# Performance work log

Measured on AMD Instinct MI355X. Metric: run time of the kernel, lower is better.

## Reference

```python
import jax, jax.numpy as jnp
import numpy as np

B, S, DIM, HEADS, DH = 1, 192, 512, 8, 64
LN_EPS = 1e-5


def setup_inputs() -> dict:
    key = jax.random.key(0)
    ks = jax.random.split(key, 5)
    rn = lambda k, shp: jax.random.normal(k, shp, dtype=jnp.float32) * 0.02
    return {
        "x": jax.random.normal(ks[0], (B, S, DIM), dtype=jnp.float32),
        "ln_w": jnp.ones((DIM,), jnp.float32),
        "ln_b": jnp.zeros((DIM,), jnp.float32),
        "W_abcde": rn(ks[1], (5 * HEADS * DH, DIM)),
        "b_abcde": jnp.zeros((5 * HEADS * DH,), jnp.float32),
        "W_K": rn(ks[2], (HEADS, DH, DH, DH)),
        "W_V": rn(ks[3], (HEADS, DH, DH, DH)),
        "W_out": rn(ks[4], (DIM, HEADS * DH)),
        "b_out": jnp.zeros((DIM,), jnp.float32),
    }


def reference(x, ln_w, ln_b, W_abcde, b_abcde, W_K, W_V, W_out, b_out):
    b, n, _ = x.shape
    # LayerNorm (biased variance, eps=1e-5, affine)
    mu = jnp.mean(x, axis=-1, keepdims=True)
    var = jnp.var(x, axis=-1, keepdims=True)
    xn = (x - mu) / jnp.sqrt(var + LN_EPS) * ln_w + ln_b
    # abcde projection, chunk into 5, split heads -> [b, n, h, d]
    proj = xn @ W_abcde.T + b_abcde
    a_, b_, c_, d_, e_ = [t.reshape(b, n, HEADS, DH) for t in jnp.split(proj, 5, axis=-1)]
    # cubic attention score chain (note: heads summed out in step2, reintroduced by a_)
    step1 = jnp.einsum('brnk,nijk->brij', c_, W_K)          # [b, r, d, d]
    step2 = jnp.einsum('brij,bqnj->briq', step1, b_)        # [b, r, d, q] (sum over heads of b_)
    attn = jnp.einsum('briq,bpni->bnpqr', step2, a_)        # [b, h, p, q, r]
    # "causal" mask: positions where p >= q set to 1e-6 (faithful to masked_fill_)
    t_idx = jnp.arange(n)[:, None, None]
    s_idx = jnp.arange(n)[None, :, None]
    mask = (t_idx >= s_idx)[None, None]                      # [1,1,p,q,1]
    attn = jnp.where(mask, jnp.float32(1e-6), attn)
    # 'b n p1 p2 p3 -> b n p3 (p1 p2)', scale by 1/dim_head, softmax over (p1 p2)
    attn = attn.transpose(0, 1, 4, 2, 3).reshape(b, HEADS, n, n * n) / DH
    attn = jax.nn.softmax(attn, axis=-1)
    # pairwise values: [b, p1, p2, h, d] -> 'b p s n h -> b n h (p s)'
    v = jnp.einsum('bpnh,bqng,nhgf->bpqnf', d_, e_, W_V)
    v = v.transpose(0, 3, 4, 1, 2).reshape(b, HEADS, DH, n * n)
    # weighted sum over pair axis, merge heads
    z = jnp.einsum('bnql,bnhl->bqnh', attn, v).reshape(b, n, HEADS * DH)
    return z @ W_out.T + b_out
```

## Files before the change

kernel.cpp:

```cpp
#include <hip/hip_runtime.h>
#include <hip/hip_bf16.h>
#include <cstdint>

#define SEQ 192

typedef float f32x4 __attribute__((ext_vector_type(4)));
typedef float f32x8 __attribute__((ext_vector_type(8)));
typedef __bf16 bf16;
typedef __bf16 bf16x8 __attribute__((ext_vector_type(8)));
typedef __bf16 bf16x4 __attribute__((ext_vector_type(4)));

#define MFMA_BF16(a, b, c) __builtin_amdgcn_mfma_f32_16x16x32_bf16(a, b, c, 0, 0, 0)

__device__ __forceinline__ bf16x8 cvt8(f32x8 v) {
  bf16x8 o;
#pragma unroll
  for (int i = 0; i < 8; i++) o[i] = (bf16)v[i];
  return o;
}

__global__ __launch_bounds__(256) void k1_prep(
    const float* __restrict__ x, const float* __restrict__ ln_w, const float* __restrict__ ln_b,
    const float* __restrict__ WV, bf16* __restrict__ xn_bf, bf16* __restrict__ WVt2) {
  int bid = blockIdx.x, tid = threadIdx.x;
  if (bid < 512) {
    int g = bid & 63, hh = bid >> 6;
    __shared__ float ld[64 * 65];
    int f = tid & 63, r4 = tid >> 6;
#pragma unroll
    for (int it = 0; it < 16; it++) {
      int hp = it * 4 + r4;
      ld[hp * 65 + f] = WV[(((size_t)(hh * 64 + hp) * 64 + g) * 64) + f];
    }
    __syncthreads();
    int hp2 = tid & 63;
#pragma unroll
    for (int it = 0; it < 16; it++) {
      int ff = it * 4 + r4;
      WVt2[(size_t)hh * 262144 + (size_t)(ff * 64 + g) * 64 + hp2] = (bf16)ld[hp2 * 65 + ff];
    }
    return;
  }
  bid -= 512;
  {
    int r = bid;
    const float* xr = x + (size_t)r * 512;
    float v0 = xr[tid], v1 = xr[tid + 256];
    float s = v0 + v1, s2 = v0 * v0 + v1 * v1;
#pragma unroll
    for (int off = 32; off > 0; off >>= 1) {
      s += __shfl_down(s, off);
      s2 += __shfl_down(s2, off);
    }
    __shared__ float redS[4], redS2[4];
    int wave = tid >> 6, lane = tid & 63;
    if (lane == 0) { redS[wave] = s; redS2[wave] = s2; }
    __syncthreads();
    float S = redS[0] + redS[1] + redS[2] + redS[3];
    float S2 = redS2[0] + redS2[1] + redS2[2] + redS2[3];
    float mean = S * (1.0f / 512.0f);
    float var = S2 * (1.0f / 512.0f) - mean * mean;
    float rstd = rsqrtf(var + 1e-5f);
    bf16* xnr = xn_bf + (size_t)r * 512;
    xnr[tid] = (bf16)((v0 - mean) * rstd * ln_w[tid] + ln_b[tid]);
    xnr[tid + 256] = (bf16)((v1 - mean) * rstd * ln_w[tid + 256] + ln_b[tid + 256]);
  }
}

template <int MODE>
__device__ __forceinline__ void gemm_body(const bf16* __restrict__ A, const bf16* __restrict__ Bt,
                                          bf16* __restrict__ C1, int N, int K,
                                          int nb, int mb, int tid) {
  int n0 = nb * 64, m0 = mb * 64;
  int wave = tid >> 6, lane = tid & 63;
  int lq = lane >> 4, l16 = lane & 15;
  const bf16* Ap = A + (size_t)(m0 + wave * 16 + l16) * K;
  f32x4 acc[4];
#pragma unroll
  for (int nt = 0; nt < 4; nt++) acc[nt] = (f32x4){0.f, 0.f, 0.f, 0.f};
  for (int k0 = 0; k0 < K; k0 += 32) {
    bf16x8 af = *(const bf16x8*)(Ap + k0 + lq * 8);
#pragma unroll
    for (int nt = 0; nt < 4; nt++) {
      bf16x8 bv = *(const bf16x8*)(Bt + (size_t)(n0 + nt * 16 + l16) * K + k0 + lq * 8);
      acc[nt] = MFMA_BF16(af, bv, acc[nt]);
    }
  }
  int cm = m0 + wave * 16 + lq * 4;
#pragma unroll
  for (int nt = 0; nt < 4; nt++) {
    int n = n0 + nt * 16 + l16;
    if constexpr (MODE == 1) {
#pragma unroll
      for (int rg = 0; rg < 4; rg++) C1[(size_t)(cm + rg) * N + n] = (bf16)acc[nt][rg];
    } else {
      int r = cm >> 6, i0 = cm & 63;
      bf16x4 pk = {(bf16)acc[nt][0], (bf16)acc[nt][1], (bf16)acc[nt][2], (bf16)acc[nt][3]};
      *(bf16x4*)(C1 + (size_t)r * 12288 + (size_t)n * 64 + i0) = pk;
    }
  }
}

__global__ __launch_bounds__(256) void k2_proj(
    const bf16* __restrict__ xn_bf, const float* __restrict__ Wab,
    const float* __restrict__ b_abcde, float* __restrict__ proj, bf16* __restrict__ a_bf,
    bf16* __restrict__ c_bf, bf16* __restrict__ d_bf) {
  int bid = blockIdx.x, tid = threadIdx.x;
  int nb = bid % 40, mb = bid / 40;
  int n0 = nb * 64, m0 = mb * 64;
  int wave = tid >> 6, lane = tid & 63;
  int lq = lane >> 4, l16 = lane & 15;
  const bf16* Ap = xn_bf + (size_t)(m0 + wave * 16 + l16) * 512;
  f32x4 acc[4];
#pragma unroll
  for (int nt = 0; nt < 4; nt++) acc[nt] = (f32x4){0.f, 0.f, 0.f, 0.f};
  for (int k0 = 0; k0 < 512; k0 += 32) {
    bf16x8 af = *(const bf16x8*)(Ap + k0 + lq * 8);
#pragma unroll
    for (int nt = 0; nt < 4; nt++) {
      f32x8 wv = *(const f32x8*)(Wab + (size_t)(n0 + nt * 16 + l16) * 512 + k0 + lq * 8);
      acc[nt] = MFMA_BF16(af, cvt8(wv), acc[nt]);
    }
  }
  int cm = m0 + wave * 16 + lq * 4;
#pragma unroll
  for (int nt = 0; nt < 4; nt++) {
    int n = n0 + nt * 16 + l16;
    int chunk = n >> 9, hcol = (n >> 6) & 7, i = n & 63;
#pragma unroll
    for (int rg = 0; rg < 4; rg++) {
      int m = cm + rg;
      float v = acc[nt][rg] + b_abcde[n];
      proj[(size_t)m * 2560 + n] = v;
      bf16 bv = (bf16)v;
      if (chunk == 0) a_bf[((size_t)hcol * SEQ + m) * 64 + i] = bv;
      else if (chunk == 2) c_bf[(size_t)m * 512 + (n - 1024)] = bv;
      else if (chunk == 3) d_bf[((size_t)hcol * SEQ + m) * 64 + i] = bv;
    }
  }
}

__global__ __launch_bounds__(256) void k3_mid(
    const bf16* __restrict__ c_bf, const float* __restrict__ WK, bf16* __restrict__ s1bf,
    const bf16* __restrict__ d_bf, const bf16* __restrict__ WVt2, bf16* __restrict__ tTt,
    const float* __restrict__ proj, bf16* __restrict__ eT_bf, float* __restrict__ ecum,
    bf16* __restrict__ bsum_bf) {
  __shared__ float el[64 * 65];
  int bid = blockIdx.x, tid = threadIdx.x;
  if (bid < 192) {
    int nb = bid % 64, mb = bid / 64;
    int n0 = nb * 64, m0 = mb * 64;
    int wave = tid >> 6, lane = tid & 63;
    int lq = lane >> 4, l16 = lane & 15;
    const bf16* Ap = c_bf + (size_t)(m0 + wave * 16 + l16) * 512;
    f32x4 acc[4];
#pragma unroll
    for (int nt = 0; nt < 4; nt++) acc[nt] = (f32x4){0.f, 0.f, 0.f, 0.f};
    size_t offn[4];
#pragma unroll
    for (int nt = 0; nt < 4; nt++) {
      int n = n0 + nt * 16 + l16;
      offn[nt] = (size_t)(n >> 6) * 4096 + (size_t)(n & 63) * 64;
    }
    for (int k0 = 0; k0 < 512; k0 += 32) {
      bf16x8 af = *(const bf16x8*)(Ap + k0 + lq * 8);
      size_t kb = (size_t)(k0 >> 6) * 262144 + (k0 & 32) + lq * 8;
#pragma unroll
      for (int nt = 0; nt < 4; nt++) {
        f32x8 wv = *(const f32x8*)(WK + kb + offn[nt]);
        acc[nt] = MFMA_BF16(af, cvt8(wv), acc[nt]);
      }
    }
    int cm = m0 + wave * 16 + lq * 4;
#pragma unroll
    for (int nt = 0; nt < 4; nt++) {
      int n = n0 + nt * 16 + l16;
#pragma unroll
      for (int rg = 0; rg < 4; rg++) s1bf[(size_t)(cm + rg) * 4096 + n] = (bf16)acc[nt][rg];
    }
    return;
  }
  bid -= 192;
  if (bid < 1536) {
    int h = bid / 192, rem = bid % 192;
    gemm_body<1>(d_bf + (size_t)h * 12288, WVt2 + (size_t)h * 262144,
                 tTt + (size_t)h * 786432, 4096, 64, rem % 64, rem / 64, tid);
    return;
  }
  bid -= 1536;
  if (bid < 8) {
    int h = bid;
    float carry = 0.f;
    for (int ch = 0; ch < 3; ch++) {
      int pbase = ch * 64;
      for (int idx = tid; idx < 4096; idx += 256) {
        int pl = idx >> 6, g = idx & 63;
        el[pl * 65 + g] = proj[(size_t)(pbase + pl) * 2560 + 2048 + h * 64 + g];
      }
      __syncthreads();
      for (int idx = tid; idx < 4096; idx += 256) {
        int g = idx >> 6, ql = idx & 63;
        eT_bf[((size_t)h * 64 + g) * SEQ + pbase + ql] = (bf16)el[ql * 65 + g];
      }
      if (tid < 64) {
        float run = carry;
        for (int pl = 0; pl < 64; pl++) {
          run += el[pl * 65 + tid];
          ecum[(size_t)h * 12288 + (pbase + pl) * 64 + tid] = run;
        }
        carry = run;
      }
      __syncthreads();
    }
    return;
  }
  bid -= 8;
  {
    int j = tid & 63, qg = tid >> 6;
#pragma unroll
    for (int qi = 0; qi < 16; qi++) {
      int q = bid * 64 + qg * 16 + qi;
      float s = 0.f;
#pragma unroll
      for (int hh = 0; hh < 8; hh++) s += proj[(size_t)q * 2560 + 512 + hh * 64 + j];
      bsum_bf[q * 64 + j] = (bf16)s;
    }
  }
}

__global__ __launch_bounds__(256) void k4_step2(const bf16* __restrict__ s1bf,
                                                const bf16* __restrict__ bsum_bf,
                                                bf16* __restrict__ s2bf) {
  int bid = blockIdx.x;
  gemm_body<2>(s1bf, bsum_bf, s2bf, 192, 64, bid % 3, bid / 3, threadIdx.x);
}

__global__ __launch_bounds__(256, 3) void k5_attn(
    const bf16* __restrict__ a_bf, const bf16* __restrict__ s2bf,
    const bf16* __restrict__ eT_bf, const float* __restrict__ ecum,
    bf16* __restrict__ ew_bf, float* __restrict__ Lsum) {
  int r = blockIdx.x, h = blockIdx.y;
  int tid = threadIdx.x, wave = tid >> 6, lane = tid & 63;
  int lq = lane >> 4, l16 = lane & 15;
  __shared__ __align__(16) bf16 wch[2][4][3][16 * 40];
  __shared__ float redL[4];
  int pt[3] = {wave, wave + 4, 11 - wave};

  const bf16* ah = a_bf + (size_t)h * 12288;
  const bf16* s2r = s2bf + (size_t)r * 12288;
  const bf16* eh = eT_bf + (size_t)h * 12288;
  const float* ech = ecum + (size_t)h * 12288;

  bf16x8 afr[3][2];
#pragma unroll
  for (int mt = 0; mt < 3; mt++)
#pragma unroll
    for (int kc = 0; kc < 2; kc++)
      afr[mt][kc] = *(const bf16x8*)(ah + (pt[mt] * 16 + l16) * 64 + kc * 32 + lq * 8);

  f32x4 ewacc[3][4];
#pragma unroll
  for (int mt = 0; mt < 3; mt++)
#pragma unroll
    for (int nt = 0; nt < 4; nt++) ewacc[mt][nt] = (f32x4){0.f, 0.f, 0.f, 0.f};
  float lpart = 0.f;

  for (int c = 0; c < 6; c++) {
    if (c * 32 + 31 <= wave * 16) continue;
    int par = c & 1;
    bf16x8 efr[4];
#pragma unroll
    for (int nt = 0; nt < 4; nt++)
      efr[nt] = *(const bf16x8*)(eh + (nt * 16 + l16) * SEQ + c * 32 + lq * 8);
    bf16x8 bq[2][2];
#pragma unroll
    for (int sub = 0; sub < 2; sub++) {
      int q = c * 32 + sub * 16 + l16;
      bq[sub][0] = *(const bf16x8*)(s2r + q * 64 + lq * 8);
      bq[sub][1] = *(const bf16x8*)(s2r + q * 64 + 32 + lq * 8);
    }
    f32x4 sacc[3][2];
#pragma unroll
    for (int mt = 0; mt < 3; mt++) {
      if (c * 32 + 31 <= pt[mt] * 16) continue;
#pragma unroll
      for (int sub = 0; sub < 2; sub++) {
        if (c * 32 + sub * 16 + 15 <= pt[mt] * 16) continue;
        f32x4 sv = (f32x4){0.f, 0.f, 0.f, 0.f};
        sv = MFMA_BF16(afr[mt][0], bq[sub][0], sv);
        sacc[mt][sub] = MFMA_BF16(afr[mt][1], bq[sub][1], sv);
      }
    }
#pragma unroll
    for (int mt = 0; mt < 3; mt++) {
      if (c * 32 + 31 <= pt[mt] * 16) continue;
      bf16* mybuf = &wch[par][wave][mt][0];
#pragma unroll
      for (int sub = 0; sub < 2; sub++) {
        if (c * 32 + sub * 16 + 15 <= pt[mt] * 16) {
#pragma unroll
          for (int rg = 0; rg < 4; rg++) mybuf[(lq * 4 + rg) * 40 + sub * 16 + l16] = (bf16)0.f;
          continue;
        }
        int q = c * 32 + sub * 16 + l16;
        int p0 = pt[mt] * 16 + lq * 4;
#pragma unroll
        for (int rg = 0; rg < 4; rg++) {
          float wv = (q > p0 + rg) ? __expf(sacc[mt][sub][rg] * 0.015625f) : 0.f;
          lpart += wv;
          mybuf[(lq * 4 + rg) * 40 + sub * 16 + l16] = (bf16)wv;
        }
      }
    }
#pragma unroll
    for (int mt = 0; mt < 3; mt++) {
      if (c * 32 + 31 <= pt[mt] * 16) continue;
      bf16x8 wf = *(const bf16x8*)(&wch[par][wave][mt][l16 * 40 + lq * 8]);
#pragma unroll
      for (int nt = 0; nt < 4; nt++) ewacc[mt][nt] = MFMA_BF16(wf, efr[nt], ewacc[mt][nt]);
    }
  }

  bf16* ewout = ew_bf + ((size_t)h * SEQ + r) * 12288;
#pragma unroll
  for (int mt = 0; mt < 3; mt++)
#pragma unroll
    for (int nt = 0; nt < 4; nt++)
#pragma unroll
      for (int rg = 0; rg < 4; rg++) {
        int p = pt[mt] * 16 + lq * 4 + rg;
        int g = nt * 16 + l16;
        ewout[p * 64 + g] = (bf16)(ewacc[mt][nt][rg] + ech[p * 64 + g]);
      }

#pragma unroll
  for (int off = 32; off > 0; off >>= 1) lpart += __shfl_down(lpart, off);
  if (lane == 0) redL[wave] = lpart;
  __syncthreads();
  if (tid == 0) Lsum[h * SEQ + r] = redL[0] + redL[1] + redL[2] + redL[3];
}

__global__ __launch_bounds__(512) void k5b_z(
    const bf16* __restrict__ ew_bf, const bf16* __restrict__ tTt, float* __restrict__ Zpart) {
  int h = blockIdx.x, mt = blockIdx.y, ks = blockIdx.z;
  int tid = threadIdx.x, wave = tid >> 6, lane = tid & 63;
  int lq = lane >> 4, l16 = lane & 15;
  __shared__ float zred[8][16][66];
  const bf16* ewh = ew_bf + ((size_t)h * SEQ + mt * 32) * 12288;
  const bf16* th = tTt + (size_t)h * 786432;
  f32x4 acc[2][4];
#pragma unroll
  for (int m2 = 0; m2 < 2; m2++)
#pragma unroll
    for (int nt = 0; nt < 4; nt++) acc[m2][nt] = (f32x4){0.f, 0.f, 0.f, 0.f};
  for (int jj = 0; jj < 6; jj++) {
    int kc = ks * 48 + wave * 6 + jj;
    int p = kc >> 1, g0 = (kc & 1) * 32;
    bf16x8 af0 = *(const bf16x8*)(ewh + (size_t)l16 * 12288 + kc * 32 + lq * 8);
    bf16x8 af1 = *(const bf16x8*)(ewh + (size_t)(16 + l16) * 12288 + kc * 32 + lq * 8);
#pragma unroll
    for (int nt = 0; nt < 4; nt++) {
      bf16x8 tf = *(const bf16x8*)(th + (size_t)p * 4096 + (nt * 16 + l16) * 64 + g0 + lq * 8);
      acc[0][nt] = MFMA_BF16(af0, tf, acc[0][nt]);
      acc[1][nt] = MFMA_BF16(af1, tf, acc[1][nt]);
    }
  }
#pragma unroll
  for (int m2 = 0; m2 < 2; m2++) {
    if (m2) __syncthreads();
#pragma unroll
    for (int nt = 0; nt < 4; nt++)
#pragma unroll
      for (int rg = 0; rg < 4; rg++) zred[wave][lq * 4 + rg][nt * 16 + l16] = acc[m2][nt][rg];
    __syncthreads();
#pragma unroll
    for (int o = 0; o < 2; o++) {
      int idx = o * 512 + tid;
      int rloc = idx >> 6, f = idx & 63;
      float s = 0.f;
#pragma unroll
      for (int wv = 0; wv < 8; wv++) s += zred[wv][rloc][f];
      Zpart[(size_t)ks * 98304 + (size_t)(mt * 32 + m2 * 16 + rloc) * 512 + h * 64 + f] = s;
    }
  }
}

__global__ __launch_bounds__(256) void k5c_zf(const float* __restrict__ Zpart,
                                              const float* __restrict__ Lsum,
                                              bf16* __restrict__ z_bf) {
  int m = blockIdx.x, tid = threadIdx.x;
#pragma unroll
  for (int o = 0; o < 2; o++) {
    int c = o * 256 + tid;
    int h = c >> 6;
    float s = 0.f;
#pragma unroll
    for (int ks = 0; ks < 8; ks++) s += Zpart[(size_t)ks * 98304 + (size_t)m * 512 + c];
    float L = Lsum[h * SEQ + m] + 18528.0f;
    z_bf[(size_t)m * 512 + c] = (bf16)(s / L);
  }
}

__global__ __launch_bounds__(256) void k6_out(
    const bf16* __restrict__ z_bf, const float* __restrict__ Wout,
    const float* __restrict__ b_out, float* __restrict__ out) {
  int bid = blockIdx.x, tid = threadIdx.x;
  int nb = bid & 7, mb = bid >> 3;
  int wave = tid >> 6, lane = tid & 63;
  int lq = lane >> 4, l16 = lane & 15;
  int m = mb * 16 + l16;
  f32x4 acc[4];
#pragma unroll
  for (int nt = 0; nt < 4; nt++) acc[nt] = (f32x4){0.f, 0.f, 0.f, 0.f};
#pragma unroll
  for (int kc = 0; kc < 4; kc++) {
    int k0 = wave * 128 + kc * 32;
    bf16x8 af = *(const bf16x8*)(z_bf + (size_t)m * 512 + k0 + lq * 8);
#pragma unroll
    for (int nt = 0; nt < 4; nt++) {
      f32x8 wv = *(const f32x8*)(Wout + (size_t)(nb * 64 + nt * 16 + l16) * 512 + k0 + lq * 8);
      acc[nt] = MFMA_BF16(af, cvt8(wv), acc[nt]);
    }
  }
  __shared__ float red[4][16][68];
#pragma unroll
  for (int nt = 0; nt < 4; nt++)
#pragma unroll
    for (int rg = 0; rg < 4; rg++) red[wave][lq * 4 + rg][nt * 16 + l16] = acc[nt][rg];
  __syncthreads();
#pragma unroll
  for (int o = 0; o < 4; o++) {
    int idx = o * 256 + tid;
    int rloc = idx >> 6, f = idx & 63;
    float s = red[0][rloc][f] + red[1][rloc][f] + red[2][rloc][f] + red[3][rloc][f];
    out[(size_t)(mb * 16 + rloc) * 512 + nb * 64 + f] = s + b_out[nb * 64 + f];
  }
}

static const size_t OFF_PROJ = 0;
static const size_t OFF_ECUM = 491520;
static const size_t OFF_XN = 589824;
static const size_t OFF_ZPART = 638976;
static const size_t OFF_LSUM = 1425408;
static const size_t OFF_Z = 1427456;
static const size_t OFF_WVT = 2473984;
static const size_t OFF_A = 3522560;
static const size_t OFF_C = 3571712;
static const size_t OFF_D = 3620864;
static const size_t OFF_ET = 3670016;
static const size_t OFF_BSUM = 3719168;
static const size_t OFF_S1 = 3725312;
static const size_t OFF_S2 = 4118528;
static const size_t OFF_TT = 5298176;
static const size_t OFF_EW = 8493056;

extern "C" void kernel_launch(void* const* d_in, const int* in_sizes, int n_in,
                              void* d_out, int out_size, void* d_ws, size_t ws_size,
                              hipStream_t stream) {
  (void)in_sizes; (void)n_in; (void)out_size; (void)ws_size;
  const float* x = (const float*)d_in[0];
  const float* ln_w = (const float*)d_in[1];
  const float* ln_b = (const float*)d_in[2];
  const float* W_abcde = (const float*)d_in[3];
  const float* b_abcde = (const float*)d_in[4];
  const float* W_K = (const float*)d_in[5];
  const float* W_V = (const float*)d_in[6];
  const float* W_out = (const float*)d_in[7];
  const float* b_out = (const float*)d_in[8];
  float* out = (float*)d_out;
  float* ws = (float*)d_ws;

  float* proj = ws + OFF_PROJ;
  float* ecum = ws + OFF_ECUM;
  bf16* xn_bf = (bf16*)(ws + OFF_XN);
  float* Zpart = ws + OFF_ZPART;
  float* Lsum = ws + OFF_LSUM;
  bf16* z_bf = (bf16*)(ws + OFF_Z);
  bf16* WVt2 = (bf16*)(ws + OFF_WVT);
  bf16* a_bf = (bf16*)(ws + OFF_A);
  bf16* c_bf = (bf16*)(ws + OFF_C);
  bf16* d_bf = (bf16*)(ws + OFF_D);
  bf16* eT_bf = (bf16*)(ws + OFF_ET);
  bf16* bsum_bf = (bf16*)(ws + OFF_BSUM);
  bf16* s1bf = (bf16*)(ws + OFF_S1);
  bf16* s2bf = (bf16*)(ws + OFF_S2);
  bf16* tTt = (bf16*)(ws + OFF_TT);
  bf16* ew_bf = (bf16*)(ws + OFF_EW);

  k1_prep<<<704, 256, 0, stream>>>(x, ln_w, ln_b, W_V, xn_bf, WVt2);
  k2_proj<<<120, 256, 0, stream>>>(xn_bf, W_abcde, b_abcde, proj, a_bf, c_bf, d_bf);
  k3_mid<<<1739, 256, 0, stream>>>(c_bf, W_K, s1bf, d_bf, WVt2, tTt, proj, eT_bf, ecum,
                                   bsum_bf);
  k4_step2<<<576, 256, 0, stream>>>(s1bf, bsum_bf, s2bf);
  k5_attn<<<dim3(SEQ, 8), 256, 0, stream>>>(a_bf, s2bf, eT_bf, ecum, ew_bf, Lsum);
  k5b_z<<<dim3(8, 6, 8), 512, 0, stream>>>(ew_bf, tTt, Zpart);
  k5c_zf<<<SEQ, 256, 0, stream>>>(Zpart, Lsum, z_bf);
  k6_out<<<96, 256, 0, stream>>>(z_bf, W_out, b_out, out);
}
```

Before: 214.9 us.

## Fuse step2 GEMM into attention kernel and z-normalize into output projection

Recomputes the s1×bsum step2 product per (r,h) block directly into shared memory inside the attention kernel, removing the separate step2 kernel and its global s2 buffer. Also merges the Zpart reduction/normalization into the output projection kernel, staging z in LDS. This cuts two launches and intermediate global traffic at the cost of redundant step2 work across heads, extra LDS per block, and dropping the double-buffered weight chunk. A missing barrier in the ecum chunk loop is also added.

```diff
diff --git a/kernel.cpp b/kernel.cpp
--- a/kernel.cpp
+++ b/kernel.cpp
@@ -67,10 +67,9 @@
   }
 }
 
-template <int MODE>
-__device__ __forceinline__ void gemm_body(const bf16* __restrict__ A, const bf16* __restrict__ Bt,
-                                          bf16* __restrict__ C1, int N, int K,
-                                          int nb, int mb, int tid) {
+__device__ __forceinline__ void gemm_rm(const bf16* __restrict__ A, const bf16* __restrict__ Bt,
+                                        bf16* __restrict__ C1, int N, int K, int nb, int mb,
+                                        int tid) {
   int n0 = nb * 64, m0 = mb * 64;
   int wave = tid >> 6, lane = tid & 63;
   int lq = lane >> 4, l16 = lane & 15;
@@ -90,14 +89,8 @@
 #pragma unroll
   for (int nt = 0; nt < 4; nt++) {
     int n = n0 + nt * 16 + l16;
-    if constexpr (MODE == 1) {
-#pragma unroll
-      for (int rg = 0; rg < 4; rg++) C1[(size_t)(cm + rg) * N + n] = (bf16)acc[nt][rg];
-    } else {
-      int r = cm >> 6, i0 = cm & 63;
-      bf16x4 pk = {(bf16)acc[nt][0], (bf16)acc[nt][1], (bf16)acc[nt][2], (bf16)acc[nt][3]};
-      *(bf16x4*)(C1 + (size_t)r * 12288 + (size_t)n * 64 + i0) = pk;
-    }
+#pragma unroll
+    for (int rg = 0; rg < 4; rg++) C1[(size_t)(cm + rg) * N + n] = (bf16)acc[nt][rg];
   }
 }
 
@@ -183,8 +176,8 @@
   bid -= 192;
   if (bid < 1536) {
     int h = bid / 192, rem = bid % 192;
-    gemm_body<1>(d_bf + (size_t)h * 12288, WVt2 + (size_t)h * 262144,
-                 tTt + (size_t)h * 786432, 4096, 64, rem % 64, rem / 64, tid);
+    gemm_rm(d_bf + (size_t)h * 12288, WVt2 + (size_t)h * 262144,
+            tTt + (size_t)h * 786432, 4096, 64, rem % 64, rem / 64, tid);
     return;
   }
   bid -= 1536;
@@ -193,6 +186,7 @@
     float carry = 0.f;
     for (int ch = 0; ch < 3; ch++) {
       int pbase = ch * 64;
+      if (ch) __syncthreads();
       for (int idx = tid; idx < 4096; idx += 256) {
         int pl = idx >> 6, g = idx & 63;
         el[pl * 65 + g] = proj[(size_t)(pbase + pl) * 2560 + 2048 + h * 64 + g];
@@ -228,26 +222,39 @@
   }
 }
 
-__global__ __launch_bounds__(256) void k4_step2(const bf16* __restrict__ s1bf,
-                                                const bf16* __restrict__ bsum_bf,
-                                                bf16* __restrict__ s2bf) {
-  int bid = blockIdx.x;
-  gemm_body<2>(s1bf, bsum_bf, s2bf, 192, 64, bid % 3, bid / 3, threadIdx.x);
-}
-
-__global__ __launch_bounds__(256, 3) void k5_attn(
-    const bf16* __restrict__ a_bf, const bf16* __restrict__ s2bf,
-    const bf16* __restrict__ eT_bf, const float* __restrict__ ecum,
-    bf16* __restrict__ ew_bf, float* __restrict__ Lsum) {
+__global__ __launch_bounds__(256, 3) void k45_attn(
+    const bf16* __restrict__ a_bf, const bf16* __restrict__ s1bf,
+    const bf16* __restrict__ bsum_bf, const bf16* __restrict__ eT_bf,
+    const float* __restrict__ ecum, bf16* __restrict__ ew_bf, float* __restrict__ Lsum) {
   int r = blockIdx.x, h = blockIdx.y;
   int tid = threadIdx.x, wave = tid >> 6, lane = tid & 63;
   int lq = lane >> 4, l16 = lane & 15;
-  __shared__ __align__(16) bf16 wch[2][4][3][16 * 40];
+  __shared__ __align__(16) bf16 s2L[SEQ * 72];
+  __shared__ __align__(16) bf16 wch[4][3][16 * 40];
   __shared__ float redL[4];
+
+  {
+    const bf16* s1r = s1bf + (size_t)r * 4096;
+    bf16x8 aS[2];
+#pragma unroll
+    for (int kc = 0; kc < 2; kc++)
+      aS[kc] = *(const bf16x8*)(s1r + (wave * 16 + l16) * 64 + kc * 32 + lq * 8);
+#pragma unroll
+    for (int qt = 0; qt < 12; qt++) {
+      f32x4 acc = (f32x4){0.f, 0.f, 0.f, 0.f};
+#pragma unroll
+      for (int kc = 0; kc < 2; kc++) {
+        bf16x8 bv = *(const bf16x8*)(bsum_bf + (qt * 16 + l16) * 64 + kc * 32 + lq * 8);
+        acc = MFMA_BF16(aS[kc], bv, acc);
+      }
+      bf16x4 pk = {(bf16)acc[0], (bf16)acc[1], (bf16)acc[2], (bf16)acc[3]};
+      *(bf16x4*)(&s2L[(qt * 16 + l16) * 72 + wave * 16 + lq * 4]) = pk;
+    }
+  }
+  __syncthreads();
+
   int pt[3] = {wave, wave + 4, 11 - wave};
-
   const bf16* ah = a_bf + (size_t)h * 12288;
-  const bf16* s2r = s2bf + (size_t)r * 12288;
   const bf16* eh = eT_bf + (size_t)h * 12288;
   const float* ech = ecum + (size_t)h * 12288;
 
@@ -265,27 +272,26 @@
     for (int nt = 0; nt < 4; nt++) ewacc[mt][nt] = (f32x4){0.f, 0.f, 0.f, 0.f};
   float lpart = 0.f;
 
-  for (int c = 0; c < 6; c++) {
-    if (c * 32 + 31 <= wave * 16) continue;
-    int par = c & 1;
+  for (int cc = 0; cc < 6; cc++) {
+    if (cc * 32 + 31 <= wave * 16) continue;
     bf16x8 efr[4];
 #pragma unroll
     for (int nt = 0; nt < 4; nt++)
-      efr[nt] = *(const bf16x8*)(eh + (nt * 16 + l16) * SEQ + c * 32 + lq * 8);
+      efr[nt] = *(const bf16x8*)(eh + (nt * 16 + l16) * SEQ + cc * 32 + lq * 8);
     bf16x8 bq[2][2];
 #pragma unroll
     for (int sub = 0; sub < 2; sub++) {
-      int q = c * 32 + sub * 16 + l16;
-      bq[sub][0] = *(const bf16x8*)(s2r + q * 64 + lq * 8);
-      bq[sub][1] = *(const bf16x8*)(s2r + q * 64 + 32 + lq * 8);
+      int q = cc * 32 + sub * 16 + l16;
+      bq[sub][0] = *(const bf16x8*)(&s2L[q * 72 + lq * 8]);
+      bq[sub][1] = *(const bf16x8*)(&s2L[q * 72 + 32 + lq * 8]);
     }
     f32x4 sacc[3][2];
 #pragma unroll
     for (int mt = 0; mt < 3; mt++) {
-      if (c * 32 + 31 <= pt[mt] * 16) continue;
+      if (cc * 32 + 31 <= pt[mt] * 16) continue;
 #pragma unroll
       for (int sub = 0; sub < 2; sub++) {
-        if (c * 32 + sub * 16 + 15 <= pt[mt] * 16) continue;
+        if (cc * 32 + sub * 16 + 15 <= pt[mt] * 16) continue;
         f32x4 sv = (f32x4){0.f, 0.f, 0.f, 0.f};
         sv = MFMA_BF16(afr[mt][0], bq[sub][0], sv);
         sacc[mt][sub] = MFMA_BF16(afr[mt][1], bq[sub][1], sv);
@@ -293,16 +299,16 @@
     }
 #pragma unroll
     for (int mt = 0; mt < 3; mt++) {
-      if (c * 32 + 31 <= pt[mt] * 16) continue;
-      bf16* mybuf = &wch[par][wave][mt][0];
+      if (cc * 32 + 31 <= pt[mt] * 16) continue;
+      bf16* mybuf = &wch[wave][mt][0];
 #pragma unroll
       for (int sub = 0; sub < 2; sub++) {
-        if (c * 32 + sub * 16 + 15 <= pt[mt] * 16) {
+        if (cc * 32 + sub * 16 + 15 <= pt[mt] * 16) {
 #pragma unroll
           for (int rg = 0; rg < 4; rg++) mybuf[(lq * 4 + rg) * 40 + sub * 16 + l16] = (bf16)0.f;
           continue;
         }
-        int q = c * 32 + sub * 16 + l16;
+        int q = cc * 32 + sub * 16 + l16;
         int p0 = pt[mt] * 16 + lq * 4;
 #pragma unroll
         for (int rg = 0; rg < 4; rg++) {
@@ -314,8 +320,8 @@
     }
 #pragma unroll
     for (int mt = 0; mt < 3; mt++) {
-      if (c * 32 + 31 <= pt[mt] * 16) continue;
-      bf16x8 wf = *(const bf16x8*)(&wch[par][wave][mt][l16 * 40 + lq * 8]);
+      if (cc * 32 + 31 <= pt[mt] * 16) continue;
+      bf16x8 wf = *(const bf16x8*)(&wch[wave][mt][l16 * 40 + lq * 8]);
 #pragma unroll
       for (int nt = 0; nt < 4; nt++) ewacc[mt][nt] = MFMA_BF16(wf, efr[nt], ewacc[mt][nt]);
     }
@@ -328,9 +334,9 @@
     for (int nt = 0; nt < 4; nt++)
 #pragma unroll
       for (int rg = 0; rg < 4; rg++) {
-        int p = pt[mt] * 16 + lq * 4 + rg;
+        int pp = pt[mt] * 16 + lq * 4 + rg;
         int g = nt * 16 + l16;
-        ewout[p * 64 + g] = (bf16)(ewacc[mt][nt][rg] + ech[p * 64 + g]);
+        ewout[pp * 64 + g] = (bf16)(ewacc[mt][nt][rg] + ech[pp * 64 + g]);
       }
 
 #pragma unroll
@@ -355,12 +361,12 @@
     for (int nt = 0; nt < 4; nt++) acc[m2][nt] = (f32x4){0.f, 0.f, 0.f, 0.f};
   for (int jj = 0; jj < 6; jj++) {
     int kc = ks * 48 + wave * 6 + jj;
-    int p = kc >> 1, g0 = (kc & 1) * 32;
+    int pp = kc >> 1, g0 = (kc & 1) * 32;
     bf16x8 af0 = *(const bf16x8*)(ewh + (size_t)l16 * 12288 + kc * 32 + lq * 8);
     bf16x8 af1 = *(const bf16x8*)(ewh + (size_t)(16 + l16) * 12288 + kc * 32 + lq * 8);
 #pragma unroll
     for (int nt = 0; nt < 4; nt++) {
-      bf16x8 tf = *(const bf16x8*)(th + (size_t)p * 4096 + (nt * 16 + l16) * 64 + g0 + lq * 8);
+      bf16x8 tf = *(const bf16x8*)(th + (size_t)pp * 4096 + (nt * 16 + l16) * 64 + g0 + lq * 8);
       acc[0][nt] = MFMA_BF16(af0, tf, acc[0][nt]);
       acc[1][nt] = MFMA_BF16(af1, tf, acc[1][nt]);
     }
@@ -385,54 +391,50 @@
   }
 }
 
-__global__ __launch_bounds__(256) void k5c_zf(const float* __restrict__ Zpart,
-                                              const float* __restrict__ Lsum,
-                                              bf16* __restrict__ z_bf) {
-  int m = blockIdx.x, tid = threadIdx.x;
-#pragma unroll
-  for (int o = 0; o < 2; o++) {
-    int c = o * 256 + tid;
-    int h = c >> 6;
+__global__ __launch_bounds__(256) void k6_out(
+    const float* __restrict__ Zpart, const float* __restrict__ Lsum,
+    const float* __restrict__ Wout, const float* __restrict__ b_out, float* __restrict__ out) {
+  int u = blockIdx.x, tid = threadIdx.x;
+  int mb = u >> 3, nb = u & 7;
+  __shared__ __align__(16) bf16 zt[16 * 520];
+  __shared__ float rd[4 * 16 * 68];
+  for (int idx = tid; idx < 8192; idx += 256) {
+    int m = idx >> 9, cc = idx & 511;
     float s = 0.f;
 #pragma unroll
-    for (int ks = 0; ks < 8; ks++) s += Zpart[(size_t)ks * 98304 + (size_t)m * 512 + c];
-    float L = Lsum[h * SEQ + m] + 18528.0f;
-    z_bf[(size_t)m * 512 + c] = (bf16)(s / L);
-  }
-}
-
-__global__ __launch_bounds__(256) void k6_out(
-    const bf16* __restrict__ z_bf, const float* __restrict__ Wout,
-    const float* __restrict__ b_out, float* __restrict__ out) {
-  int bid = blockIdx.x, tid = threadIdx.x;
-  int nb = bid & 7, mb = bid >> 3;
+    for (int ks = 0; ks < 8; ks++)
+      s += Zpart[(size_t)ks * 98304 + (size_t)(mb * 16 + m) * 512 + cc];
+    float L = Lsum[(cc >> 6) * SEQ + mb * 16 + m] + 18528.0f;
+    zt[m * 520 + cc] = (bf16)(s / L);
+  }
+  __syncthreads();
   int wave = tid >> 6, lane = tid & 63;
   int lq = lane >> 4, l16 = lane & 15;
-  int m = mb * 16 + l16;
   f32x4 acc[4];
 #pragma unroll
   for (int nt = 0; nt < 4; nt++) acc[nt] = (f32x4){0.f, 0.f, 0.f, 0.f};
 #pragma unroll
   for (int kc = 0; kc < 4; kc++) {
     int k0 = wave * 128 + kc * 32;
-    bf16x8 af = *(const bf16x8*)(z_bf + (size_t)m * 512 + k0 + lq * 8);
+    bf16x8 af = *(const bf16x8*)(zt + l16 * 520 + k0 + lq * 8);
 #pragma unroll
     for (int nt = 0; nt < 4; nt++) {
       f32x8 wv = *(const f32x8*)(Wout + (size_t)(nb * 64 + nt * 16 + l16) * 512 + k0 + lq * 8);
       acc[nt] = MFMA_BF16(af, cvt8(wv), acc[nt]);
     }
   }
-  __shared__ float red[4][16][68];
 #pragma unroll
   for (int nt = 0; nt < 4; nt++)
 #pragma unroll
-    for (int rg = 0; rg < 4; rg++) red[wave][lq * 4 + rg][nt * 16 + l16] = acc[nt][rg];
+    for (int rg = 0; rg < 4; rg++)
+      rd[(wave * 16 + lq * 4 + rg) * 68 + nt * 16 + l16] = acc[nt][rg];
   __syncthreads();
 #pragma unroll
   for (int o = 0; o < 4; o++) {
     int idx = o * 256 + tid;
     int rloc = idx >> 6, f = idx & 63;
-    float s = red[0][rloc][f] + red[1][rloc][f] + red[2][rloc][f] + red[3][rloc][f];
+    float s = rd[rloc * 68 + f] + rd[(16 + rloc) * 68 + f] + rd[(32 + rloc) * 68 + f] +
+              rd[(48 + rloc) * 68 + f];
     out[(size_t)(mb * 16 + rloc) * 512 + nb * 64 + f] = s + b_out[nb * 64 + f];
   }
 }
@@ -440,19 +442,17 @@
 static const size_t OFF_PROJ = 0;
 static const size_t OFF_ECUM = 491520;
 static const size_t OFF_XN = 589824;
-static const size_t OFF_ZPART = 638976;
-static const size_t OFF_LSUM = 1425408;
-static const size_t OFF_Z = 1427456;
-static const size_t OFF_WVT = 2473984;
-static const size_t OFF_A = 3522560;
-static const size_t OFF_C = 3571712;
-static const size_t OFF_D = 3620864;
-static const size_t OFF_ET = 3670016;
-static const size_t OFF_BSUM = 3719168;
-static const size_t OFF_S1 = 3725312;
-static const size_t OFF_S2 = 4118528;
-static const size_t OFF_TT = 5298176;
-static const size_t OFF_EW = 8493056;
+static const size_t OFF_LSUM = 638976;
+static const size_t OFF_ZPART = 640512;
+static const size_t OFF_WVT = 2213376;
+static const size_t OFF_A = 3261952;
+static const size_t OFF_C = 3311104;
+static const size_t OFF_D = 3360256;
+static const size_t OFF_ET = 3409408;
+static const size_t OFF_BSUM = 3458560;
+static const size_t OFF_S1 = 3464704;
+static const size_t OFF_TT = 5037568;
+static const size_t OFF_EW = 8183296;
 
 extern "C" void kernel_launch(void* const* d_in, const int* in_sizes, int n_in,
                               void* d_out, int out_size, void* d_ws, size_t ws_size,
@@ -473,9 +473,8 @@
   float* proj = ws + OFF_PROJ;
   float* ecum = ws + OFF_ECUM;
   bf16* xn_bf = (bf16*)(ws + OFF_XN);
+  float* Lsum = ws + OFF_LSUM;
   float* Zpart = ws + OFF_ZPART;
-  float* Lsum = ws + OFF_LSUM;
-  bf16* z_bf = (bf16*)(ws + OFF_Z);
   bf16* WVt2 = (bf16*)(ws + OFF_WVT);
   bf16* a_bf = (bf16*)(ws + OFF_A);
   bf16* c_bf = (bf16*)(ws + OFF_C);
@@ -483,7 +482,6 @@
   bf16* eT_bf = (bf16*)(ws + OFF_ET);
   bf16* bsum_bf = (bf16*)(ws + OFF_BSUM);
   bf16* s1bf = (bf16*)(ws + OFF_S1);
-  bf16* s2bf = (bf16*)(ws + OFF_S2);
   bf16* tTt = (bf16*)(ws + OFF_TT);
   bf16* ew_bf = (bf16*)(ws + OFF_EW);
 
@@ -491,9 +489,7 @@
   k2_proj<<<120, 256, 0, stream>>>(xn_bf, W_abcde, b_abcde, proj, a_bf, c_bf, d_bf);
   k3_mid<<<1739, 256, 0, stream>>>(c_bf, W_K, s1bf, d_bf, WVt2, tTt, proj, eT_bf, ecum,
                                    bsum_bf);
-  k4_step2<<<576, 256, 0, stream>>>(s1bf, bsum_bf, s2bf);
-  k5_attn<<<dim3(SEQ, 8), 256, 0, stream>>>(a_bf, s2bf, eT_bf, ecum, ew_bf, Lsum);
+  k45_attn<<<dim3(SEQ, 8), 256, 0, stream>>>(a_bf, s1bf, bsum_bf, eT_bf, ecum, ew_bf, Lsum);
   k5b_z<<<dim3(8, 6, 8), 512, 0, stream>>>(ew_bf, tTt, Zpart);
-  k5c_zf<<<SEQ, 256, 0, stream>>>(Zpart, Lsum, z_bf);
-  k6_out<<<96, 256, 0, stream>>>(z_bf, W_out, b_out, out);
-}
+  k6_out<<<96, 256, 0, stream>>>(Zpart, Lsum, W_out, b_out, out);
+}
```

Result: slower. 221.0 us (+2.9%).
